# Kernel optimization log

Measured on AMD Instinct MI355X. Metric: run time of the kernel, lower is better.

## Reference

```python
import jax, jax.numpy as jnp
import numpy as np

LATENT = 128
LN_EPS = 1e-3  # keras LayerNormalization default epsilon


def _mlp(x, W0, b0, W1, b1, W2, b2, gamma, beta):
    # two relu hidden layers + linear output + layer norm (MeshGraphNets style)
    h = jax.nn.relu(x @ W0 + b0)
    h = jax.nn.relu(h @ W1 + b1)
    h = h @ W2 + b2
    mu = jnp.mean(h, axis=-1, keepdims=True)
    var = jnp.var(h, axis=-1, keepdims=True)
    return (h - mu) * jax.lax.rsqrt(var + LN_EPS) * gamma + beta


def setup_inputs() -> dict:
    key = jax.random.key(0)
    ks = jax.random.split(key, 12)
    N, D, E = 10000, 128, 320000
    cat = 3 * D  # sender + receiver + edge features concatenated
    s = lambda fan: 1.0 / np.sqrt(fan)
    return {
        "sender_features": jax.random.normal(ks[0], (N, D), jnp.float32),
        "receiver_features": jax.random.normal(ks[1], (N, D), jnp.float32),
        "edge_features": jax.random.normal(ks[2], (E, D), jnp.float32),
        "senders": jax.random.randint(ks[3], (E,), 0, N, jnp.int32),
        "receivers": jax.random.randint(ks[4], (E,), 0, N, jnp.int32),
        "W0": jax.random.normal(ks[5], (cat, LATENT), jnp.float32) * s(cat),
        "b0": jnp.zeros((LATENT,), jnp.float32),
        "W1": jax.random.normal(ks[6], (LATENT, LATENT), jnp.float32) * s(LATENT),
        "b1": jnp.zeros((LATENT,), jnp.float32),
        "W2": jax.random.normal(ks[7], (LATENT, LATENT), jnp.float32) * s(LATENT),
        "b2": jnp.zeros((LATENT,), jnp.float32),
        "gamma": jnp.ones((LATENT,), jnp.float32),
        "beta": jnp.zeros((LATENT,), jnp.float32),
    }


def reference(sender_features, receiver_features, edge_features, senders,
              receivers, W0, b0, W1, b1, W2, b2, gamma, beta):
    g_send = jnp.take(sender_features, senders, axis=0)      # [E, D]
    g_recv = jnp.take(receiver_features, receivers, axis=0)  # [E, D]
    feats = jnp.concatenate([g_send, g_recv, edge_features], axis=-1)  # [E, 3D]
    return _mlp(feats, W0, b0, W1, b1, W2, b2, gamma, beta)  # [E, LATENT]
```

## Files before the change

kernel.cpp:

```cpp
#include <hip/hip_runtime.h>
#include <stdint.h>


typedef __attribute__((ext_vector_type(8))) short   s16x8;
typedef __attribute__((ext_vector_type(8))) __bf16  bf16x8;
typedef __attribute__((ext_vector_type(4))) float   f32x4;
typedef __attribute__((ext_vector_type(4))) int     i32x4;

__device__ __forceinline__ unsigned rne_bf16(float x) {
  unsigned u = __builtin_bit_cast(unsigned, x);
  return (u + 0x7fffu + ((u >> 16) & 1u)) >> 16;
}

__device__ __forceinline__ f32x4 mfma_bf16(s16x8 a, s16x8 b, f32x4 c) {
  return __builtin_amdgcn_mfma_f32_16x16x32_bf16(
      __builtin_bit_cast(bf16x8, a), __builtin_bit_cast(bf16x8, b), c, 0, 0, 0);
}

__device__ __forceinline__ void split8(float4 a, float4 b, s16x8 &hi, s16x8 &lo) {
  float v[8] = {a.x, a.y, a.z, a.w, b.x, b.y, b.z, b.w};
#pragma unroll
  for (int j = 0; j < 8; ++j) {
    unsigned hb = rne_bf16(v[j]);
    float fh = __builtin_bit_cast(float, hb << 16);
    unsigned lb = rne_bf16(v[j] - fh);
    hi[j] = (short)hb;
    lo[j] = (short)lb;
  }
}

__device__ __forceinline__ void stage_slab(const short *__restrict__ base,
                                           int planeElems, int K, int slab,
                                           char *sB, int tid) {
#pragma unroll
  for (int i = 0; i < 4; ++i) {
    int c   = tid + i * 512;
    int p   = c >> 10;
    int c10 = c & 1023;
    int n   = c10 >> 3;
    int kc  = c10 & 7;
    i32x4 v = *(const i32x4 *)(base + p * planeElems + n * K + slab * 64 + kc * 8);
    *(i32x4 *)(sB + p * 16384 + n * 128 + ((kc ^ (n & 7)) << 4)) = v;
  }
}

__device__ __forceinline__ void do_kstep(const char *sB, int kc, int lr,
                                         s16x8 ah, s16x8 al, f32x4 (&acc)[8]) {
#pragma unroll
  for (int nt = 0; nt < 8; ++nt) {
    int n    = nt * 16 + lr;
    int boff = n * 128 + ((kc ^ (n & 7)) << 4);
    s16x8 bh = *(const s16x8 *)(sB + boff);
    s16x8 bl = *(const s16x8 *)(sB + 16384 + boff);
    acc[nt] = mfma_bf16(ah, bh, acc[nt]);
    acc[nt] = mfma_bf16(al, bh, acc[nt]);
    acc[nt] = mfma_bf16(ah, bl, acc[nt]);
  }
}

__device__ __forceinline__ void write_h(char *sH, const float *__restrict__ bias,
                                        int lr, int lg, f32x4 (&acc)[8]) {
#pragma unroll
  for (int nt = 0; nt < 8; ++nt) {
    int c = nt * 16 + lr;
    float bv = bias[c];
#pragma unroll
    for (int j = 0; j < 4; ++j) {
      float h = fmaxf(acc[nt][j] + bv, 0.0f);
      unsigned hb = rne_bf16(h);
      float fh = __builtin_bit_cast(float, hb << 16);
      unsigned lb = rne_bf16(h - fh);
      int hr   = lg * 4 + j;
      int boff = hr * 256 + (((c >> 3) ^ (hr & 7)) << 4) + (c & 7) * 2;
      *(short *)(sH + boff)        = (short)hb;
      *(short *)(sH + 4096 + boff) = (short)lb;
    }
  }
}

__global__ void prep_weights(const float *__restrict__ W0,
                             const float *__restrict__ W1,
                             const float *__restrict__ W2,
                             short *__restrict__ ws) {
  int idx = blockIdx.x * 256 + threadIdx.x;
  const float *W;
  int K, off, rel, plane;
  if (idx < 49152)      { W = W0; K = 384; off = 0;      rel = idx;         plane = 49152; }
  else if (idx < 65536) { W = W1; K = 128; off = 98304;  rel = idx - 49152; plane = 16384; }
  else                  { W = W2; K = 128; off = 131072; rel = idx - 65536; plane = 16384; }
  int n = rel / K;
  int k = rel - n * K;
  float v = W[(size_t)k * 128 + n];
  unsigned hb = rne_bf16(v);
  float fh = __builtin_bit_cast(float, hb << 16);
  unsigned lb = rne_bf16(v - fh);
  ws[off + rel]         = (short)hb;
  ws[off + plane + rel] = (short)lb;
}

__global__ __launch_bounds__(512, 2) void edge_mlp(
    const float *__restrict__ sf, const float *__restrict__ rf,
    const float *__restrict__ ef, const int *__restrict__ snd,
    const int *__restrict__ rcv, const short *__restrict__ wt,
    const float *__restrict__ b0, const float *__restrict__ b1,
    const float *__restrict__ b2, const float *__restrict__ gamma,
    const float *__restrict__ beta, float *__restrict__ out) {
  __shared__ __align__(16) char lds[131072];
  const int tid  = threadIdx.x;
  const int wave = tid >> 6;
  const int lane = tid & 63;
  const int lr   = lane & 15;
  const int lg   = lane >> 4;
  const int arow = blockIdx.x * 128 + wave * 16 + lr;
  const int sidx = snd[arow];
  const int ridx = rcv[arow];

  char *sB0 = lds;
  char *sB1 = lds + 32768;
  char *sH  = lds + 65536 + wave * 8192;

  const f32x4 fz = {0.f, 0.f, 0.f, 0.f};
  f32x4 acc[8];
#pragma unroll
  for (int i = 0; i < 8; ++i) acc[i] = fz;

  stage_slab(wt, 49152, 384, 0, sB0, tid);
  __syncthreads();
#pragma unroll
  for (int s = 0; s < 6; ++s) {
    const float *ab;
    if (s < 2)      ab = sf + (size_t)sidx * 128 + s * 64;
    else if (s < 4) ab = rf + (size_t)ridx * 128 + (s - 2) * 64;
    else            ab = ef + (size_t)arow * 128 + (s - 4) * 64;
    float4 x0 = *(const float4 *)(ab + lg * 8);
    float4 x1 = *(const float4 *)(ab + lg * 8 + 4);
    float4 x2 = *(const float4 *)(ab + 32 + lg * 8);
    float4 x3 = *(const float4 *)(ab + 32 + lg * 8 + 4);
    if (s < 5) stage_slab(wt, 49152, 384, s + 1, (s & 1) ? sB0 : sB1, tid);
    const char *cur = (s & 1) ? sB1 : sB0;
    s16x8 ah, al;
    split8(x0, x1, ah, al);
    do_kstep(cur, lg, lr, ah, al, acc);
    split8(x2, x3, ah, al);
    do_kstep(cur, 4 + lg, lr, ah, al, acc);
    __syncthreads();
  }
  write_h(sH, b0, lr, lg, acc);

#pragma unroll
  for (int i = 0; i < 8; ++i) acc[i] = fz;
  stage_slab(wt + 98304, 16384, 128, 0, sB0, tid);
  __syncthreads();
#pragma unroll
  for (int s = 0; s < 2; ++s) {
    if (s < 1) stage_slab(wt + 98304, 16384, 128, 1, sB1, tid);
    const char *cur = (s & 1) ? sB1 : sB0;
#pragma unroll
    for (int ks = 0; ks < 2; ++ks) {
      int kch  = s * 8 + ks * 4 + lg;
      int aoff = lr * 256 + ((kch ^ (lr & 7)) << 4);
      s16x8 ah = *(const s16x8 *)(sH + aoff);
      s16x8 al = *(const s16x8 *)(sH + 4096 + aoff);
      do_kstep(cur, ks * 4 + lg, lr, ah, al, acc);
    }
    __syncthreads();
  }
  write_h(sH, b1, lr, lg, acc);

#pragma unroll
  for (int i = 0; i < 8; ++i) acc[i] = fz;
  stage_slab(wt + 131072, 16384, 128, 0, sB0, tid);
  __syncthreads();
#pragma unroll
  for (int s = 0; s < 2; ++s) {
    if (s < 1) stage_slab(wt + 131072, 16384, 128, 1, sB1, tid);
    const char *cur = (s & 1) ? sB1 : sB0;
#pragma unroll
    for (int ks = 0; ks < 2; ++ks) {
      int kch  = s * 8 + ks * 4 + lg;
      int aoff = lr * 256 + ((kch ^ (lr & 7)) << 4);
      s16x8 ah = *(const s16x8 *)(sH + aoff);
      s16x8 al = *(const s16x8 *)(sH + 4096 + aoff);
      do_kstep(cur, ks * 4 + lg, lr, ah, al, acc);
    }
    __syncthreads();
  }

  float hv[8][4];
  float sum[4] = {0.f, 0.f, 0.f, 0.f}, sq[4] = {0.f, 0.f, 0.f, 0.f};
#pragma unroll
  for (int nt = 0; nt < 8; ++nt) {
    int c = nt * 16 + lr;
    float bv = b2[c];
#pragma unroll
    for (int j = 0; j < 4; ++j) {
      float v = acc[nt][j] + bv;
      hv[nt][j] = v;
      sum[j] += v;
      sq[j]  += v * v;
    }
  }
#pragma unroll
  for (int m = 1; m < 16; m <<= 1) {
#pragma unroll
    for (int j = 0; j < 4; ++j) {
      sum[j] += __shfl_xor(sum[j], m, 64);
      sq[j]  += __shfl_xor(sq[j], m, 64);
    }
  }
  float mu[4], rs[4];
#pragma unroll
  for (int j = 0; j < 4; ++j) {
    mu[j] = sum[j] * (1.0f / 128.0f);
    float var = sq[j] * (1.0f / 128.0f) - mu[j] * mu[j];
    rs[j] = rsqrtf(var + 1e-3f);
  }
  const int orow = blockIdx.x * 128 + wave * 16 + lg * 4;
#pragma unroll
  for (int nt = 0; nt < 8; ++nt) {
    int c = nt * 16 + lr;
    float g  = gamma[c];
    float bt = beta[c];
#pragma unroll
    for (int j = 0; j < 4; ++j) {
      out[(size_t)(orow + j) * 128 + c] = (hv[nt][j] - mu[j]) * rs[j] * g + bt;
    }
  }
}

extern "C" void kernel_launch(void* const* d_in, const int* in_sizes, int n_in,
                              void* d_out, int out_size, void* d_ws, size_t ws_size,
                              hipStream_t stream) {
  const float *sf    = (const float *)d_in[0];
  const float *rf    = (const float *)d_in[1];
  const float *ef    = (const float *)d_in[2];
  const int   *snd   = (const int *)d_in[3];
  const int   *rcv   = (const int *)d_in[4];
  const float *W0    = (const float *)d_in[5];
  const float *b0    = (const float *)d_in[6];
  const float *W1    = (const float *)d_in[7];
  const float *b1    = (const float *)d_in[8];
  const float *W2    = (const float *)d_in[9];
  const float *b2    = (const float *)d_in[10];
  const float *gamma = (const float *)d_in[11];
  const float *beta  = (const float *)d_in[12];
  short *wt = (short *)d_ws;

  prep_weights<<<320, 256, 0, stream>>>(W0, W1, W2, wt);
  edge_mlp<<<2500, 512, 0, stream>>>(sf, rf, ef, snd, rcv, wt,
                                     b0, b1, b2, gamma, beta, (float *)d_out);
}
```

Baseline: 498.3 us.

## Switch to single-pass fp16 32x32 MFMA with register-resident hidden activations

New measurement: 426.2 us. 14.5% less time.

```diff
diff --git a/kernel.cpp b/kernel.cpp
--- a/kernel.cpp
+++ b/kernel.cpp
@@ -2,251 +2,230 @@
 #include <stdint.h>
 
 
-typedef __attribute__((ext_vector_type(8))) short   s16x8;
-typedef __attribute__((ext_vector_type(8))) __bf16  bf16x8;
-typedef __attribute__((ext_vector_type(4))) float   f32x4;
-typedef __attribute__((ext_vector_type(4))) int     i32x4;
-
-__device__ __forceinline__ unsigned rne_bf16(float x) {
-  unsigned u = __builtin_bit_cast(unsigned, x);
-  return (u + 0x7fffu + ((u >> 16) & 1u)) >> 16;
-}
-
-__device__ __forceinline__ f32x4 mfma_bf16(s16x8 a, s16x8 b, f32x4 c) {
-  return __builtin_amdgcn_mfma_f32_16x16x32_bf16(
-      __builtin_bit_cast(bf16x8, a), __builtin_bit_cast(bf16x8, b), c, 0, 0, 0);
-}
-
-__device__ __forceinline__ void split8(float4 a, float4 b, s16x8 &hi, s16x8 &lo) {
-  float v[8] = {a.x, a.y, a.z, a.w, b.x, b.y, b.z, b.w};
+typedef __attribute__((ext_vector_type(8)))  short    s16x8;
+typedef __attribute__((ext_vector_type(8)))  _Float16 f16x8;
+typedef __attribute__((ext_vector_type(16))) float    f32x16;
+typedef __attribute__((ext_vector_type(4)))  float    f32x4;
+
+__device__ __forceinline__ f32x16 mfma16(f16x8 a, f16x8 b, f32x16 c) {
+  return __builtin_amdgcn_mfma_f32_32x32x16_f16(a, b, c, 0, 0, 0);
+}
+
+__global__ void prep_weights(const float* __restrict__ W0,
+                             const float* __restrict__ W1,
+                             const float* __restrict__ W2,
+                             short* __restrict__ ws) {
+  int tid = blockIdx.x * 256 + threadIdx.x;
+  const float* W;
+  int rel, imgbase, perm;
+  if (tid < 6144)      { W = W0; rel = tid;        imgbase = 0;     perm = 0; }
+  else if (tid < 8192) { W = W1; rel = tid - 6144; imgbase = 49152; perm = 1; }
+  else                 { W = W2; rel = tid - 8192; imgbase = 65536; perm = 1; }
+  int n     = rel & 127;
+  int chunk = rel >> 7;
+  int slab  = chunk >> 3;
+  int kc    = chunk & 7;
+  s16x8 o;
 #pragma unroll
   for (int j = 0; j < 8; ++j) {
-    unsigned hb = rne_bf16(v[j]);
-    float fh = __builtin_bit_cast(float, hb << 16);
-    unsigned lb = rne_bf16(v[j] - fh);
-    hi[j] = (short)hb;
-    lo[j] = (short)lb;
-  }
-}
-
-__device__ __forceinline__ void stage_slab(const short *__restrict__ base,
-                                           int planeElems, int K, int slab,
-                                           char *sB, int tid) {
-#pragma unroll
-  for (int i = 0; i < 4; ++i) {
-    int c   = tid + i * 512;
-    int p   = c >> 10;
-    int c10 = c & 1023;
-    int n   = c10 >> 3;
-    int kc  = c10 & 7;
-    i32x4 v = *(const i32x4 *)(base + p * planeElems + n * K + slab * 64 + kc * 8);
-    *(i32x4 *)(sB + p * 16384 + n * 128 + ((kc ^ (n & 7)) << 4)) = v;
-  }
-}
-
-__device__ __forceinline__ void do_kstep(const char *sB, int kc, int lr,
-                                         s16x8 ah, s16x8 al, f32x4 (&acc)[8]) {
-#pragma unroll
-  for (int nt = 0; nt < 8; ++nt) {
-    int n    = nt * 16 + lr;
-    int boff = n * 128 + ((kc ^ (n & 7)) << 4);
-    s16x8 bh = *(const s16x8 *)(sB + boff);
-    s16x8 bl = *(const s16x8 *)(sB + 16384 + boff);
-    acc[nt] = mfma_bf16(ah, bh, acc[nt]);
-    acc[nt] = mfma_bf16(al, bh, acc[nt]);
-    acc[nt] = mfma_bf16(ah, bl, acc[nt]);
-  }
-}
-
-__device__ __forceinline__ void write_h(char *sH, const float *__restrict__ bias,
-                                        int lr, int lg, f32x4 (&acc)[8]) {
-#pragma unroll
-  for (int nt = 0; nt < 8; ++nt) {
-    int c = nt * 16 + lr;
-    float bv = bias[c];
-#pragma unroll
-    for (int j = 0; j < 4; ++j) {
-      float h = fmaxf(acc[nt][j] + bv, 0.0f);
-      unsigned hb = rne_bf16(h);
-      float fh = __builtin_bit_cast(float, hb << 16);
-      unsigned lb = rne_bf16(h - fh);
-      int hr   = lg * 4 + j;
-      int boff = hr * 256 + (((c >> 3) ^ (hr & 7)) << 4) + (c & 7) * 2;
-      *(short *)(sH + boff)        = (short)hb;
-      *(short *)(sH + 4096 + boff) = (short)lb;
-    }
-  }
-}
-
-__global__ void prep_weights(const float *__restrict__ W0,
-                             const float *__restrict__ W1,
-                             const float *__restrict__ W2,
-                             short *__restrict__ ws) {
-  int idx = blockIdx.x * 256 + threadIdx.x;
-  const float *W;
-  int K, off, rel, plane;
-  if (idx < 49152)      { W = W0; K = 384; off = 0;      rel = idx;         plane = 49152; }
-  else if (idx < 65536) { W = W1; K = 128; off = 98304;  rel = idx - 49152; plane = 16384; }
-  else                  { W = W2; K = 128; off = 131072; rel = idx - 65536; plane = 16384; }
-  int n = rel / K;
-  int k = rel - n * K;
-  float v = W[(size_t)k * 128 + n];
-  unsigned hb = rne_bf16(v);
-  float fh = __builtin_bit_cast(float, hb << 16);
-  unsigned lb = rne_bf16(v - fh);
-  ws[off + rel]         = (short)hb;
-  ws[off + plane + rel] = (short)lb;
-}
-
-__global__ __launch_bounds__(512, 2) void edge_mlp(
-    const float *__restrict__ sf, const float *__restrict__ rf,
-    const float *__restrict__ ef, const int *__restrict__ snd,
-    const int *__restrict__ rcv, const short *__restrict__ wt,
-    const float *__restrict__ b0, const float *__restrict__ b1,
-    const float *__restrict__ b2, const float *__restrict__ gamma,
-    const float *__restrict__ beta, float *__restrict__ out) {
-  __shared__ __align__(16) char lds[131072];
-  const int tid  = threadIdx.x;
-  const int wave = tid >> 6;
+    int kslot = slab * 64 + kc * 8 + j;
+    int ktrue = perm ? ((kslot & ~12) | ((kslot & 4) << 1) | ((kslot & 8) >> 1))
+                     : kslot;
+    float v = W[(size_t)ktrue * 128 + n];
+    o[j] = __builtin_bit_cast(short, (_Float16)v);
+  }
+  *(s16x8*)(ws + imgbase + slab * 8192 + n * 64 + ((kc ^ (n & 7)) << 3)) = o;
+}
+
+__device__ __forceinline__ void stage(const short* __restrict__ ws, int s,
+                                      char* lds, int tid) {
+  char* buf = lds + (s & 3) * 16384;
+  const char* g = (const char*)ws + s * 16384;
+#pragma unroll
+  for (int i = 0; i < 2; ++i) {
+    char* lp = buf + (i * 512 + (tid & ~63)) * 16;
+    const char* gp = g + (i * 512 + tid) * 16;
+    __builtin_amdgcn_global_load_lds(
+        (__attribute__((address_space(1))) const void*)gp,
+        (__attribute__((address_space(3))) void*)lp, 16, 0, 0);
+  }
+}
+
+__device__ __forceinline__ void kstep(const char* buf, int q, int lg1,
+                                      int e31, f16x8 xf, f32x16* acc) {
+  const int kc = q * 2 + lg1;
+  const int slot = (kc ^ (e31 & 7)) << 4;
+#pragma unroll
+  for (int nt = 0; nt < 4; ++nt) {
+    int n = nt * 32 + e31;
+    s16x8 wf = *(const s16x8*)(buf + n * 128 + slot);
+    acc[nt] = mfma16(__builtin_bit_cast(f16x8, wf), xf, acc[nt]);
+  }
+}
+
+__device__ __forceinline__ void transition(const float* __restrict__ b,
+                                           int lg1, f32x16* acc, f16x8* fr) {
+#pragma unroll
+  for (int ks = 0; ks < 8; ++ks) {
+    const int nt = ks >> 1;
+#pragma unroll
+    for (int jq = 0; jq < 2; ++jq) {
+      int nb = nt * 32 + 16 * (ks & 1) + 8 * jq + 4 * lg1;
+      f32x4 bv = *(const f32x4*)(b + nb);
+#pragma unroll
+      for (int r = 0; r < 4; ++r) {
+        float h = acc[nt][8 * (ks & 1) + jq * 4 + r] + bv[r];
+        fr[ks][jq * 4 + r] = (_Float16)fmaxf(h, 0.0f);
+      }
+    }
+  }
+}
+
+__device__ __forceinline__ void zero_acc(f32x16* acc) {
+#pragma unroll
+  for (int nt = 0; nt < 4; ++nt)
+#pragma unroll
+    for (int i = 0; i < 16; ++i) acc[nt][i] = 0.0f;
+}
+
+__global__ __launch_bounds__(512, 4) void edge_mlp(
+    const float* __restrict__ sf, const float* __restrict__ rf,
+    const float* __restrict__ ef, const int* __restrict__ snd,
+    const int* __restrict__ rcv, const short* __restrict__ wt,
+    const float* __restrict__ b0, const float* __restrict__ b1,
+    const float* __restrict__ b2, const float* __restrict__ gamma,
+    const float* __restrict__ beta, float* __restrict__ out) {
+  __shared__ __align__(16) char lds[65536];
+  const int tid = threadIdx.x;
+  const int w   = tid >> 6;
   const int lane = tid & 63;
-  const int lr   = lane & 15;
-  const int lg   = lane >> 4;
-  const int arow = blockIdx.x * 128 + wave * 16 + lr;
-  const int sidx = snd[arow];
-  const int ridx = rcv[arow];
-
-  char *sB0 = lds;
-  char *sB1 = lds + 32768;
-  char *sH  = lds + 65536 + wave * 8192;
-
-  const f32x4 fz = {0.f, 0.f, 0.f, 0.f};
-  f32x4 acc[8];
-#pragma unroll
-  for (int i = 0; i < 8; ++i) acc[i] = fz;
-
-  stage_slab(wt, 49152, 384, 0, sB0, tid);
+  const int e31 = lane & 31;
+  const int lg1 = lane >> 5;
+  const int e   = blockIdx.x * 256 + w * 32 + e31;
+  const int sidx = snd[e];
+  const int ridx = rcv[e];
+
+  const float* xbase0 = sf + (size_t)sidx * 128 + lg1 * 8;
+  const float* xbase1 = rf + (size_t)ridx * 128 + lg1 * 8;
+  const float* xbase2 = ef + (size_t)e    * 128 + lg1 * 8;
+
+#define XPTR(t) ((t) < 8 ? xbase0 + (t) * 16 \
+                : (t) < 16 ? xbase1 + ((t) - 8) * 16 \
+                : xbase2 + ((t) - 16) * 16)
+
+  f32x16 acc[4];
+  zero_acc(acc);
+  f32x4 xa[24], xb[24];
+
+  stage(wt, 0, lds, tid);
+  stage(wt, 1, lds, tid);
+  { const float* p0 = XPTR(0); xa[0] = *(const f32x4*)p0; xb[0] = *(const f32x4*)(p0 + 4);
+    const float* p1 = XPTR(1); xa[1] = *(const f32x4*)p1; xb[1] = *(const f32x4*)(p1 + 4); }
   __syncthreads();
+
 #pragma unroll
   for (int s = 0; s < 6; ++s) {
-    const float *ab;
-    if (s < 2)      ab = sf + (size_t)sidx * 128 + s * 64;
-    else if (s < 4) ab = rf + (size_t)ridx * 128 + (s - 2) * 64;
-    else            ab = ef + (size_t)arow * 128 + (s - 4) * 64;
-    float4 x0 = *(const float4 *)(ab + lg * 8);
-    float4 x1 = *(const float4 *)(ab + lg * 8 + 4);
-    float4 x2 = *(const float4 *)(ab + 32 + lg * 8);
-    float4 x3 = *(const float4 *)(ab + 32 + lg * 8 + 4);
-    if (s < 5) stage_slab(wt, 49152, 384, s + 1, (s & 1) ? sB0 : sB1, tid);
-    const char *cur = (s & 1) ? sB1 : sB0;
-    s16x8 ah, al;
-    split8(x0, x1, ah, al);
-    do_kstep(cur, lg, lr, ah, al, acc);
-    split8(x2, x3, ah, al);
-    do_kstep(cur, 4 + lg, lr, ah, al, acc);
+    stage(wt, s + 2, lds, tid);
+    const char* buf = lds + (s & 3) * 16384;
+#pragma unroll
+    for (int q = 0; q < 4; ++q) {
+      const int t = s * 4 + q;
+      if (t + 2 < 24) {
+        const float* p = XPTR(t + 2);
+        xa[t + 2] = *(const f32x4*)p;
+        xb[t + 2] = *(const f32x4*)(p + 4);
+      }
+      f16x8 xf;
+#pragma unroll
+      for (int j = 0; j < 4; ++j) {
+        xf[j]     = (_Float16)xa[t][j];
+        xf[4 + j] = (_Float16)xb[t][j];
+      }
+      kstep(buf, q, lg1, e31, xf, acc);
+    }
     __syncthreads();
   }
-  write_h(sH, b0, lr, lg, acc);
-
-#pragma unroll
-  for (int i = 0; i < 8; ++i) acc[i] = fz;
-  stage_slab(wt + 98304, 16384, 128, 0, sB0, tid);
-  __syncthreads();
-#pragma unroll
-  for (int s = 0; s < 2; ++s) {
-    if (s < 1) stage_slab(wt + 98304, 16384, 128, 1, sB1, tid);
-    const char *cur = (s & 1) ? sB1 : sB0;
-#pragma unroll
-    for (int ks = 0; ks < 2; ++ks) {
-      int kch  = s * 8 + ks * 4 + lg;
-      int aoff = lr * 256 + ((kch ^ (lr & 7)) << 4);
-      s16x8 ah = *(const s16x8 *)(sH + aoff);
-      s16x8 al = *(const s16x8 *)(sH + 4096 + aoff);
-      do_kstep(cur, ks * 4 + lg, lr, ah, al, acc);
-    }
+
+  f16x8 fr[8];
+  transition(b0, lg1, acc, fr);
+  zero_acc(acc);
+
+#pragma unroll
+  for (int s = 6; s < 8; ++s) {
+    stage(wt, s + 2, lds, tid);
+    const char* buf = lds + (s & 3) * 16384;
+#pragma unroll
+    for (int q = 0; q < 4; ++q) kstep(buf, q, lg1, e31, fr[(s - 6) * 4 + q], acc);
     __syncthreads();
   }
-  write_h(sH, b1, lr, lg, acc);
-
-#pragma unroll
-  for (int i = 0; i < 8; ++i) acc[i] = fz;
-  stage_slab(wt + 131072, 16384, 128, 0, sB0, tid);
-  __syncthreads();
-#pragma unroll
-  for (int s = 0; s < 2; ++s) {
-    if (s < 1) stage_slab(wt + 131072, 16384, 128, 1, sB1, tid);
-    const char *cur = (s & 1) ? sB1 : sB0;
-#pragma unroll
-    for (int ks = 0; ks < 2; ++ks) {
-      int kch  = s * 8 + ks * 4 + lg;
-      int aoff = lr * 256 + ((kch ^ (lr & 7)) << 4);
-      s16x8 ah = *(const s16x8 *)(sH + aoff);
-      s16x8 al = *(const s16x8 *)(sH + 4096 + aoff);
-      do_kstep(cur, ks * 4 + lg, lr, ah, al, acc);
-    }
-    __syncthreads();
-  }
-
-  float hv[8][4];
-  float sum[4] = {0.f, 0.f, 0.f, 0.f}, sq[4] = {0.f, 0.f, 0.f, 0.f};
-#pragma unroll
-  for (int nt = 0; nt < 8; ++nt) {
-    int c = nt * 16 + lr;
-    float bv = b2[c];
-#pragma unroll
-    for (int j = 0; j < 4; ++j) {
-      float v = acc[nt][j] + bv;
-      hv[nt][j] = v;
-      sum[j] += v;
-      sq[j]  += v * v;
-    }
-  }
-#pragma unroll
-  for (int m = 1; m < 16; m <<= 1) {
-#pragma unroll
-    for (int j = 0; j < 4; ++j) {
-      sum[j] += __shfl_xor(sum[j], m, 64);
-      sq[j]  += __shfl_xor(sq[j], m, 64);
-    }
-  }
-  float mu[4], rs[4];
-#pragma unroll
-  for (int j = 0; j < 4; ++j) {
-    mu[j] = sum[j] * (1.0f / 128.0f);
-    float var = sq[j] * (1.0f / 128.0f) - mu[j] * mu[j];
-    rs[j] = rsqrtf(var + 1e-3f);
-  }
-  const int orow = blockIdx.x * 128 + wave * 16 + lg * 4;
-#pragma unroll
-  for (int nt = 0; nt < 8; ++nt) {
-    int c = nt * 16 + lr;
-    float g  = gamma[c];
-    float bt = beta[c];
-#pragma unroll
-    for (int j = 0; j < 4; ++j) {
-      out[(size_t)(orow + j) * 128 + c] = (hv[nt][j] - mu[j]) * rs[j] * g + bt;
-    }
-  }
+
+  transition(b1, lg1, acc, fr);
+  zero_acc(acc);
+
+#pragma unroll
+  for (int s = 8; s < 10; ++s) {
+    const char* buf = lds + (s & 3) * 16384;
+#pragma unroll
+    for (int q = 0; q < 4; ++q) kstep(buf, q, lg1, e31, fr[(s - 8) * 4 + q], acc);
+  }
+
+  float sum = 0.0f, sq = 0.0f;
+#pragma unroll
+  for (int nt = 0; nt < 4; ++nt)
+#pragma unroll
+    for (int qq = 0; qq < 4; ++qq) {
+      int nb = nt * 32 + qq * 8 + 4 * lg1;
+      f32x4 bv = *(const f32x4*)(b2 + nb);
+#pragma unroll
+      for (int r = 0; r < 4; ++r) {
+        float v = acc[nt][qq * 4 + r] + bv[r];
+        acc[nt][qq * 4 + r] = v;
+        sum += v;
+        sq  += v * v;
+      }
+    }
+  sum += __shfl_xor(sum, 32, 64);
+  sq  += __shfl_xor(sq, 32, 64);
+  const float mu  = sum * (1.0f / 128.0f);
+  const float var = sq * (1.0f / 128.0f) - mu * mu;
+  const float rs  = rsqrtf(var + 1e-3f);
+
+  float* op = out + (size_t)e * 128;
+#pragma unroll
+  for (int nt = 0; nt < 4; ++nt)
+#pragma unroll
+    for (int qq = 0; qq < 4; ++qq) {
+      int nb = nt * 32 + qq * 8 + 4 * lg1;
+      f32x4 g  = *(const f32x4*)(gamma + nb);
+      f32x4 bt = *(const f32x4*)(beta + nb);
+      f32x4 o;
+#pragma unroll
+      for (int r = 0; r < 4; ++r)
+        o[r] = (acc[nt][qq * 4 + r] - mu) * rs * g[r] + bt[r];
+      *(f32x4*)(op + nb) = o;
+    }
+#undef XPTR
 }
 
 extern "C" void kernel_launch(void* const* d_in, const int* in_sizes, int n_in,
                               void* d_out, int out_size, void* d_ws, size_t ws_size,
                               hipStream_t stream) {
-  const float *sf    = (const float *)d_in[0];
-  const float *rf    = (const float *)d_in[1];
-  const float *ef    = (const float *)d_in[2];
-  const int   *snd   = (const int *)d_in[3];
-  const int   *rcv   = (const int *)d_in[4];
-  const float *W0    = (const float *)d_in[5];
-  const float *b0    = (const float *)d_in[6];
-  const float *W1    = (const float *)d_in[7];
-  const float *b1    = (const float *)d_in[8];
-  const float *W2    = (const float *)d_in[9];
-  const float *b2    = (const float *)d_in[10];
-  const float *gamma = (const float *)d_in[11];
-  const float *beta  = (const float *)d_in[12];
-  short *wt = (short *)d_ws;
-
-  prep_weights<<<320, 256, 0, stream>>>(W0, W1, W2, wt);
-  edge_mlp<<<2500, 512, 0, stream>>>(sf, rf, ef, snd, rcv, wt,
-                                     b0, b1, b2, gamma, beta, (float *)d_out);
-}
+  const float* sf    = (const float*)d_in[0];
+  const float* rf    = (const float*)d_in[1];
+  const float* ef    = (const float*)d_in[2];
+  const int*   snd   = (const int*)d_in[3];
+  const int*   rcv   = (const int*)d_in[4];
+  const float* W0    = (const float*)d_in[5];
+  const float* b0    = (const float*)d_in[6];
+  const float* W1    = (const float*)d_in[7];
+  const float* b1    = (const float*)d_in[8];
+  const float* W2    = (const float*)d_in[9];
+  const float* b2    = (const float*)d_in[10];
+  const float* gamma = (const float*)d_in[11];
+  const float* beta  = (const float*)d_in[12];
+  short* wt = (short*)d_ws;
+
+  prep_weights<<<40, 256, 0, stream>>>(W0, W1, W2, wt);
+  edge_mlp<<<1250, 512, 0, stream>>>(sf, rf, ef, snd, rcv, wt,
+                                     b0, b1, b2, gamma, beta, (float*)d_out);
+}
```
